# Optimization experiments

Hardware: AMD Instinct MI355X
Metric: run time of the kernel (lower is better)

The kernel has to match this reference:

```python
import jax, jax.numpy as jnp
import numpy as np
from jax import lax

EPS = 1e-6


def layernorm2d(x, w, b):
    # channel LayerNorm over dim C of NCHW (biased variance), matching LayerNormFunction
    mu = jnp.mean(x, axis=1, keepdims=True)
    var = jnp.mean((x - mu) ** 2, axis=1, keepdims=True)
    y = (x - mu) * lax.rsqrt(var + EPS)
    return w[None, :, None, None] * y + b[None, :, None, None]


def conv1x1(x, W, b):
    # x: (N,C,H,W), W: (O,C), b: (O,)
    return jnp.einsum('nchw,oc->nohw', x, W) + b[None, :, None, None]


def conv3x3(x, W, b):
    # W: (O,I,3,3)
    y = lax.conv_general_dilated(x, W, window_strides=(1, 1), padding='SAME',
                                 dimension_numbers=('NCHW', 'OIHW', 'NCHW'))
    return y + b[None, :, None, None]


def avg_pool3x3(x):
    # torch F.avg_pool2d k=3, s=1, p=1, count_include_pad=True -> always divide by 9
    s = lax.reduce_window(x, 0.0, lax.add, (1, 1, 3, 3), (1, 1, 1, 1),
                          [(0, 0), (0, 0), (1, 1), (1, 1)])
    return s / 9.0


def setup_inputs() -> dict:
    key = jax.random.key(0)
    N, C, H, W = 8, 64, 128, 256
    ks = jax.random.split(key, 12)
    d = {
        'x_l': jax.random.normal(ks[0], (N, C, H, W), jnp.float32),
        'x_r': jax.random.normal(ks[1], (N, C, H, W), jnp.float32),
        'nl_w': jnp.ones((C,), jnp.float32),
        'nl_b': jnp.zeros((C,), jnp.float32),
        'nr_w': jnp.ones((C,), jnp.float32),
        'nr_b': jnp.zeros((C,), jnp.float32),
        'Wq_l': jax.random.normal(ks[2], (C, C), jnp.float32) * 0.05,
        'bq_l': jax.random.normal(ks[3], (C,), jnp.float32) * 0.05,
        'Wq_r': jax.random.normal(ks[4], (C, C), jnp.float32) * 0.05,
        'bq_r': jax.random.normal(ks[5], (C,), jnp.float32) * 0.05,
        'Wv_r': jax.random.normal(ks[6], (C, C), jnp.float32) * 0.05,
        'bv_r': jax.random.normal(ks[7], (C,), jnp.float32) * 0.05,
        'beta': jax.random.normal(ks[8], (1, C, 1, 1), jnp.float32) * 0.1,
        'gamma': jax.random.normal(ks[9], (1, C, 1, 1), jnp.float32) * 0.1,
        'W_hf': jax.random.normal(ks[10], (C, C, 3, 3), jnp.float32) * 0.02,
        'b_hf': jax.random.normal(ks[11], (C,), jnp.float32) * 0.02,
    }
    return d


def reference(x_l, x_r, nl_w, nl_b, nr_w, nr_b, Wq_l, bq_l, Wq_r, bq_r,
              Wv_r, bv_r, beta, gamma, W_hf, b_hf):
    C = x_l.shape[1]
    scale = C ** (-0.5)

    # Projections (1x1 convs); Q_l, Q_r, V_r as (N,H,W,C)
    Q_l = jnp.transpose(conv1x1(layernorm2d(x_l, nl_w, nl_b), Wq_l, bq_l), (0, 2, 3, 1))
    Q_r = jnp.transpose(conv1x1(layernorm2d(x_r, nr_w, nr_b), Wq_r, bq_r), (0, 2, 3, 1))
    V_r = jnp.transpose(conv1x1(x_r, Wv_r, bv_r), (0, 2, 3, 1))

    # Per-scanline cross attention: (N,H,W,W)
    attn = jnp.einsum('nhwc,nhvc->nhwv', Q_l, Q_r) * scale
    attn = jax.nn.softmax(attn, axis=-1)
    F_r2l = jnp.einsum('nhwv,nhvc->nhwc', attn, V_r)  # (N,H,W,C)
    F_r2l = jnp.transpose(F_r2l, (0, 3, 1, 2)) * beta  # (N,C,H,W)

    # High-frequency branch
    hf = conv3x3(x_r - avg_pool3x3(x_r), W_hf, b_hf)

    return x_l + F_r2l + gamma * hf
```

## Files before the change

### kernel.cpp

```cpp
#include <hip/hip_runtime.h>
#include <hip/hip_bf16.h>

#define N_ 8
#define C_ 64
#define H_ 128
#define W_ 256
#define HW_ (H_*W_)
#define CHW_ (C_*H_*W_)

typedef unsigned int u32;
typedef unsigned short u16;
typedef float f32x4 __attribute__((ext_vector_type(4)));
typedef short bf16x8 __attribute__((ext_vector_type(8)));

__device__ __forceinline__ float blo(u32 u) { return __uint_as_float(u << 16); }
__device__ __forceinline__ float bhi(u32 u) { return __uint_as_float(u & 0xffff0000u); }
__device__ __forceinline__ u16 f2bf(float f) {
    u32 u = __float_as_uint(f);
    u32 lsb = (u >> 16) & 1u;
    u += 0x7fffu + lsb;
    return (u16)(u >> 16);
}
__device__ __forceinline__ u32 pack2(float a, float b) {
    return (u32)f2bf(a) | ((u32)f2bf(b) << 16);
}
__device__ __forceinline__ int rmap(int px) {
    return (px & 0xF8) | ((px + (px >> 3)) & 7);
}

__global__ __launch_bounds__(512, 2) void k_fused(
    const float* __restrict__ xl, const float* __restrict__ xr,
    const float* __restrict__ nlw, const float* __restrict__ nlb,
    const float* __restrict__ nrw, const float* __restrict__ nrb,
    const float* __restrict__ Wql, const float* __restrict__ bql,
    const float* __restrict__ Wqr, const float* __restrict__ bqr,
    const float* __restrict__ Wvr, const float* __restrict__ bvr,
    const float* __restrict__ beta, float* __restrict__ out)
{
    __shared__ u32 B1[8192];
    __shared__ u32 B2[8192];
    __shared__ float muA[256], rsA[256];
    __shared__ float SlA[64], BlA[64], SrA[64], BrA[64], BvA[64];
    const int tid  = threadIdx.x;
    const int lane = tid & 63, wv = tid >> 6;
    const int l15  = lane & 15, kg = lane >> 4;
    const int mw   = wv & 3;
    const int nh   = wv >> 2;
    const int blk  = blockIdx.x;
    const int n = blk >> 7, h = blk & 127;
    const size_t gbase = (size_t)n*CHW_ + (size_t)h*W_;

    if (tid < 64) {
        const int o = tid;
        float sl = 0.f, bl = bql[o], sr = 0.f, br = bqr[o];
        for (int c = 0; c < 64; ++c) {
            float wl = Wql[o*64+c], wr = Wqr[o*64+c];
            sl += wl * nlw[c];
            bl += wl * nlb[c];
            sr += wr * nrw[c];
            br += wr * nrb[c];
        }
        SlA[o] = sl; BlA[o] = bl; SrA[o] = sr; BrA[o] = br; BvA[o] = bvr[o];
    }

    const int oA = mw*16 + l15;
    bf16x8 aL[2], aR[2], aV[2];
    #pragma unroll
    for (int hf = 0; hf < 2; ++hf) {
        bf16x8 tl, tr, tv;
        #pragma unroll
        for (int j = 0; j < 8; ++j) {
            const int c = hf*32 + kg*8 + j;
            tl[j] = (short)f2bf(Wql[oA*64+c] * nlw[c]);
            tr[j] = (short)f2bf(Wqr[oA*64+c] * nrw[c]);
            tv[j] = (short)f2bf(Wvr[oA*64+c]);
        }
        aL[hf] = tl; aR[hf] = tr; aV[hf] = tv;
    }

    const int schunk = tid >> 6;
    const int sj     = tid & 63;

    {
        const int c0 = schunk*8;
        float4 v[8];
        #pragma unroll
        for (int e = 0; e < 8; ++e)
            v[e] = *(const float4*)(xl + gbase + (size_t)(c0+e)*HW_ + sj*4);
        #pragma unroll
        for (int t = 0; t < 4; ++t) {
            const int px = sj*4 + t;
            const int r = rmap(px);
            u32 q0,q1,q2,q3;
            const float* f0 = (const float*)&v[0]; const float* f1 = (const float*)&v[1];
            const float* f2 = (const float*)&v[2]; const float* f3 = (const float*)&v[3];
            const float* f4 = (const float*)&v[4]; const float* f5 = (const float*)&v[5];
            const float* f6 = (const float*)&v[6]; const float* f7 = (const float*)&v[7];
            asm("v_cvt_pk_bf16_f32 %0, %1, %2" : "=v"(q0) : "v"(f0[t]), "v"(f1[t]));
            asm("v_cvt_pk_bf16_f32 %0, %1, %2" : "=v"(q1) : "v"(f2[t]), "v"(f3[t]));
            asm("v_cvt_pk_bf16_f32 %0, %1, %2" : "=v"(q2) : "v"(f4[t]), "v"(f5[t]));
            asm("v_cvt_pk_bf16_f32 %0, %1, %2" : "=v"(q3) : "v"(f6[t]), "v"(f7[t]));
            uint4 pv; pv.x=q0; pv.y=q1; pv.z=q2; pv.w=q3;
            *(uint4*)&B1[r*32 + ((schunk ^ (r&7))<<2)] = pv;
        }
    }
    float4 vr2[8];
    {
        const int c0 = schunk*8;
        #pragma unroll
        for (int e = 0; e < 8; ++e)
            vr2[e] = *(const float4*)(xr + gbase + (size_t)(c0+e)*HW_ + sj*4);
    }
    __syncthreads();
    if (tid < 256) {
        const int px = tid;
        const int r = rmap(px);
        float sum = 0.f, ssq = 0.f;
        #pragma unroll
        for (int c8 = 0; c8 < 8; ++c8) {
            uint4 val = *(const uint4*)&B1[r*32 + ((c8 ^ (r&7))<<2)];
            const u32* wp = (const u32*)&val;
            #pragma unroll
            for (int q = 0; q < 4; ++q) {
                float a = blo(wp[q]), b = bhi(wp[q]);
                sum += a + b; ssq += a*a + b*b;
            }
        }
        float mu = sum * (1.f/64.f);
        float var = ssq * (1.f/64.f) - mu*mu;
        muA[px] = mu;
        rsA[px] = rsqrtf(var + 1e-6f);
    }
    __syncthreads();
    {
        float Sv[4], Bv[4];
        #pragma unroll
        for (int r4 = 0; r4 < 4; ++r4) {
            Sv[r4] = SlA[mw*16 + kg*4 + r4];
            Bv[r4] = BlA[mw*16 + kg*4 + r4];
        }
        #pragma unroll
        for (int nt2 = 0; nt2 < 8; ++nt2) {
            const int nt = nh*8 + nt2;
            const int px = nt*16 + l15;
            const int r = rmap(px);
            f32x4 d = {0.f,0.f,0.f,0.f};
            #pragma unroll
            for (int hf = 0; hf < 2; ++hf) {
                bf16x8 b = *(const bf16x8*)&B1[r*32 + (((hf*4+kg) ^ (r&7))<<2)];
                d = __builtin_amdgcn_mfma_f32_16x16x32_bf16(aL[hf], b, d, 0, 0, 0);
            }
            const float mu = muA[px], rs = rsA[px];
            uint2 pv;
            pv.x = pack2(rs*(d[0] - mu*Sv[0]) + Bv[0], rs*(d[1] - mu*Sv[1]) + Bv[1]);
            pv.y = pack2(rs*(d[2] - mu*Sv[2]) + Bv[2], rs*(d[3] - mu*Sv[3]) + Bv[3]);
            const int ci = (mw*2 + (kg>>1)) ^ (px & 7);
            *(uint2*)&B2[px*32 + (ci<<2) + (kg&1)*2] = pv;
        }
    }
    __syncthreads();

    bf16x8 qf[2][2];
    #pragma unroll
    for (int ntq = 0; ntq < 2; ++ntq)
        #pragma unroll
        for (int ci = 0; ci < 2; ++ci) {
            const int q = wv*32 + ntq*16 + l15;
            qf[ntq][ci] = *(const bf16x8*)&B2[q*32 + (((ci*4+kg) ^ (q&7))<<2)];
        }
    {
        #pragma unroll
        for (int t = 0; t < 4; ++t) {
            const int px = sj*4 + t;
            const int r = rmap(px);
            u32 q0,q1,q2,q3;
            const float* f0 = (const float*)&vr2[0]; const float* f1 = (const float*)&vr2[1];
            const float* f2 = (const float*)&vr2[2]; const float* f3 = (const float*)&vr2[3];
            const float* f4 = (const float*)&vr2[4]; const float* f5 = (const float*)&vr2[5];
            const float* f6 = (const float*)&vr2[6]; const float* f7 = (const float*)&vr2[7];
            asm("v_cvt_pk_bf16_f32 %0, %1, %2" : "=v"(q0) : "v"(f0[t]), "v"(f1[t]));
            asm("v_cvt_pk_bf16_f32 %0, %1, %2" : "=v"(q1) : "v"(f2[t]), "v"(f3[t]));
            asm("v_cvt_pk_bf16_f32 %0, %1, %2" : "=v"(q2) : "v"(f4[t]), "v"(f5[t]));
            asm("v_cvt_pk_bf16_f32 %0, %1, %2" : "=v"(q3) : "v"(f6[t]), "v"(f7[t]));
            uint4 pv; pv.x=q0; pv.y=q1; pv.z=q2; pv.w=q3;
            *(uint4*)&B1[r*32 + ((schunk ^ (r&7))<<2)] = pv;
        }
    }
    __syncthreads();
    if (tid < 256) {
        const int px = tid;
        const int r = rmap(px);
        float sum = 0.f, ssq = 0.f;
        #pragma unroll
        for (int c8 = 0; c8 < 8; ++c8) {
            uint4 val = *(const uint4*)&B1[r*32 + ((c8 ^ (r&7))<<2)];
            const u32* wp = (const u32*)&val;
            #pragma unroll
            for (int q = 0; q < 4; ++q) {
                float a = blo(wp[q]), b = bhi(wp[q]);
                sum += a + b; ssq += a*a + b*b;
            }
        }
        float mu = sum * (1.f/64.f);
        float var = ssq * (1.f/64.f) - mu*mu;
        muA[px] = mu;
        rsA[px] = rsqrtf(var + 1e-6f);
    }
    __syncthreads();

    u32 hq[8][2], hv[8][2];
    {
        float Sv[4], Bv[4];
        #pragma unroll
        for (int r4 = 0; r4 < 4; ++r4) {
            Sv[r4] = SrA[mw*16 + kg*4 + r4];
            Bv[r4] = BrA[mw*16 + kg*4 + r4];
        }
        const int chv = mw*16 + l15;
        const float vbias = BvA[chv];
        #pragma unroll
        for (int nt2 = 0; nt2 < 8; ++nt2) {
            const int nt = nh*8 + nt2;
            const int px = nt*16 + l15;
            const int r = rmap(px);
            bf16x8 bX[2];
            #pragma unroll
            for (int hf = 0; hf < 2; ++hf)
                bX[hf] = *(const bf16x8*)&B1[r*32 + (((hf*4+kg) ^ (r&7))<<2)];
            f32x4 dq = {0.f,0.f,0.f,0.f};
            f32x4 dv = {0.f,0.f,0.f,0.f};
            #pragma unroll
            for (int hf = 0; hf < 2; ++hf) {
                dq = __builtin_amdgcn_mfma_f32_16x16x32_bf16(aR[hf], bX[hf], dq, 0, 0, 0);
                dv = __builtin_amdgcn_mfma_f32_16x16x32_bf16(bX[hf], aV[hf], dv, 0, 0, 0);
            }
            const float mu = muA[px], rs = rsA[px];
            hq[nt2][0] = pack2(rs*(dq[0] - mu*Sv[0]) + Bv[0], rs*(dq[1] - mu*Sv[1]) + Bv[1]);
            hq[nt2][1] = pack2(rs*(dq[2] - mu*Sv[2]) + Bv[2], rs*(dq[3] - mu*Sv[3]) + Bv[3]);
            hv[nt2][0] = pack2(dv[0] + vbias, dv[1] + vbias);
            hv[nt2][1] = pack2(dv[2] + vbias, dv[3] + vbias);
        }
    }
    __syncthreads();
    {
        const int chv = mw*16 + l15;
        u16* Vts16 = (u16*)B2;
        #pragma unroll
        for (int nt2 = 0; nt2 < 8; ++nt2) {
            const int nt = nh*8 + nt2;
            const int px = nt*16 + l15;
            const int ciq = (mw*2 + (kg>>1)) ^ (px & 7);
            uint2 pq; pq.x = hq[nt2][0]; pq.y = hq[nt2][1];
            *(uint2*)&B1[px*32 + (ciq<<2) + (kg&1)*2] = pq;
            uint2 pw; pw.x = hv[nt2][0]; pw.y = hv[nt2][1];
            const int swz = (nt*2 + (kg>>1)) ^ (chv & 7);
            *(uint2*)&Vts16[chv*256 + (swz<<3) + (kg&1)*4] = pw;
        }
    }
    __syncthreads();

    f32x4 oacc[2][4];
    #pragma unroll
    for (int a = 0; a < 2; ++a)
        #pragma unroll
        for (int b = 0; b < 4; ++b)
            oacc[a][b] = (f32x4){0.f,0.f,0.f,0.f};
    float lsum[2] = {0.f,0.f};
    const uint4* KsR = (const uint4*)B1;
    const u16* Vts = (const u16*)B2;
    const int srcA = ((2*kg) & 3)*16 + l15;

    for (int kb = 0; kb < 8; ++kb) {
        f32x4 st[2][2];
        #pragma unroll
        for (int mt = 0; mt < 2; ++mt)
            #pragma unroll
            for (int nt = 0; nt < 2; ++nt)
                st[mt][nt] = (f32x4){0.f,0.f,0.f,0.f};
        #pragma unroll
        for (int ci = 0; ci < 2; ++ci) {
            bf16x8 a0 = *(const bf16x8*)&KsR[(kb*32 +      l15)*8 + ((ci*4 + kg) ^ (l15 & 7))];
            bf16x8 a1 = *(const bf16x8*)&KsR[(kb*32 + 16 + l15)*8 + ((ci*4 + kg) ^ (l15 & 7))];
            #pragma unroll
            for (int nt = 0; nt < 2; ++nt) {
                st[0][nt] = __builtin_amdgcn_mfma_f32_16x16x32_bf16(a0, qf[nt][ci], st[0][nt], 0, 0, 0);
                st[1][nt] = __builtin_amdgcn_mfma_f32_16x16x32_bf16(a1, qf[nt][ci], st[1][nt], 0, 0, 0);
            }
        }
        bf16x8 paR[2];
        #pragma unroll
        for (int nt = 0; nt < 2; ++nt) {
            float p00 = __expf(st[0][nt][0]*0.125f);
            float p01 = __expf(st[0][nt][1]*0.125f);
            float p02 = __expf(st[0][nt][2]*0.125f);
            float p03 = __expf(st[0][nt][3]*0.125f);
            float p10 = __expf(st[1][nt][0]*0.125f);
            float p11 = __expf(st[1][nt][1]*0.125f);
            float p12 = __expf(st[1][nt][2]*0.125f);
            float p13 = __expf(st[1][nt][3]*0.125f);
            lsum[nt] += ((p00+p01)+(p02+p03)) + ((p10+p11)+(p12+p13));
            u32 pk00, pk01, pk10, pk11;
            asm("v_cvt_pk_bf16_f32 %0, %1, %2" : "=v"(pk00) : "v"(p00), "v"(p01));
            asm("v_cvt_pk_bf16_f32 %0, %1, %2" : "=v"(pk01) : "v"(p02), "v"(p03));
            asm("v_cvt_pk_bf16_f32 %0, %1, %2" : "=v"(pk10) : "v"(p10), "v"(p11));
            asm("v_cvt_pk_bf16_f32 %0, %1, %2" : "=v"(pk11) : "v"(p12), "v"(p13));
            int a00 = __shfl((int)pk00, srcA, 64);
            int a01 = __shfl((int)pk01, srcA, 64);
            int a10 = __shfl((int)pk10, srcA, 64);
            int a11 = __shfl((int)pk11, srcA, 64);
            int b00 = __shfl((int)pk00, srcA + 16, 64);
            int b01 = __shfl((int)pk01, srcA + 16, 64);
            int b10 = __shfl((int)pk10, srcA + 16, 64);
            int b11 = __shfl((int)pk11, srcA + 16, 64);
            const bool lo = (kg < 2);
            union { u32 u[4]; bf16x8 v; } pu;
            pu.u[0] = (u32)(lo ? a00 : a10);
            pu.u[1] = (u32)(lo ? a01 : a11);
            pu.u[2] = (u32)(lo ? b00 : b10);
            pu.u[3] = (u32)(lo ? b01 : b11);
            paR[nt] = pu.v;
        }
        bf16x8 vb[4];
        #pragma unroll
        for (int nc = 0; nc < 4; ++nc)
            vb[nc] = *(const bf16x8*)&Vts[(nc*16 + l15)*256 + ((kb*4 + kg) ^ (l15 & 7))*8];
        #pragma unroll
        for (int qt = 0; qt < 2; ++qt)
            #pragma unroll
            for (int nc = 0; nc < 4; ++nc)
                oacc[qt][nc] = __builtin_amdgcn_mfma_f32_16x16x32_bf16(paR[qt], vb[nc], oacc[qt][nc], 0, 0, 0);
    }

    #pragma unroll
    for (int nt = 0; nt < 2; ++nt) {
        float s = lsum[nt];
        s += __shfl_xor(s, 16, 64);
        s += __shfl_xor(s, 32, 64);
        lsum[nt] = s;
    }
    float linv[2][4];
    #pragma unroll
    for (int qt = 0; qt < 2; ++qt)
        #pragma unroll
        for (int r = 0; r < 4; ++r)
            linv[qt][r] = 1.0f / __shfl(lsum[qt], kg*4 + r, 64);

    const size_t qbase = gbase + wv*32;
    #pragma unroll
    for (int nc = 0; nc < 4; ++nc) {
        const int ch = nc*16 + l15;
        const float bch = beta[ch];
        #pragma unroll
        for (int qt = 0; qt < 2; ++qt) {
            const size_t gidx = qbase + (size_t)ch*HW_ + qt*16 + kg*4;
            f32x4 x4 = *(const f32x4*)&xl[gidx];
            f32x4 vals;
            #pragma unroll
            for (int r = 0; r < 4; ++r)
                vals[r] = x4[r] + bch*(oacc[qt][nc][r]*linv[qt][r]);
            *(f32x4*)&out[gidx] = vals;
        }
    }
}

__global__ __launch_bounds__(256) void k_hipass(
    const float* __restrict__ xr, u16* __restrict__ Tt)
{
    __shared__ u16 Ts[64*256];
    const int bid = blockIdx.x;
    const int blk = (bid & 7)*128 + (bid >> 3);
    const int n = blk >> 7, h = blk & 127;
    const int tid = threadIdx.x;
    const int lane = tid & 63, wv = tid >> 6;
    const float* rowp = xr + (size_t)n*CHW_ + (size_t)h*W_ + lane*4;

    #pragma unroll
    for (int ci = 0; ci < 16; ++ci) {
        const int c = wv*16 + ci;
        const float* pc = rowp + (size_t)c*HW_;
        float ctr0=0.f, ctr1=0.f, ctr2=0.f, ctr3=0.f;
        float s0=0.f, s1=0.f, s2=0.f, s3=0.f;
        #pragma unroll
        for (int dy = -1; dy <= 1; ++dy) {
            const int hh = h + dy;
            float4 v = {0.f,0.f,0.f,0.f};
            if (hh >= 0 && hh < 128) v = *(const float4*)(pc + dy*W_);
            float lft = __shfl_up(v.w, 1);
            float rgt = __shfl_down(v.x, 1);
            if (lane == 0)  lft = 0.f;
            if (lane == 63) rgt = 0.f;
            s0 += lft + v.x + v.y;
            s1 += v.x + v.y + v.z;
            s2 += v.y + v.z + v.w;
            s3 += v.z + v.w + rgt;
            if (dy == 0) { ctr0=v.x; ctr1=v.y; ctr2=v.z; ctr3=v.w; }
        }
        uint2 pv;
        pv.x = pack2(ctr0 - s0*(1.f/9.f), ctr1 - s1*(1.f/9.f));
        pv.y = pack2(ctr2 - s2*(1.f/9.f), ctr3 - s3*(1.f/9.f));
        const int swz = (c >> 3) << 3;
        *(uint2*)&Ts[c*256 + ((lane*4) ^ swz)] = pv;
    }
    __syncthreads();
    uint4* gout = (uint4*)(Tt + (size_t)blk*256*64);
    #pragma unroll
    for (int iter = 0; iter < 8; ++iter) {
        const int lin = iter*256 + tid;
        const int px = lin >> 3, chunk = lin & 7;
        const int pxs = px ^ (chunk << 3);
        u32 w4[4];
        #pragma unroll
        for (int tp = 0; tp < 4; ++tp) {
            const int c0 = chunk*8 + tp*2;
            u16 a = Ts[(c0    )*256 + pxs];
            u16 b = Ts[(c0 + 1)*256 + pxs];
            w4[tp] = (u32)a | ((u32)b << 16);
        }
        uint4 v; v.x=w4[0]; v.y=w4[1]; v.z=w4[2]; v.w=w4[3];
        gout[lin] = v;
    }
}

__device__ __forceinline__ void conv_tile(
    const uint4* __restrict__ buf, const bf16x8* A,
    const float* gv, const float* bv,
    int n, int h, int w0, int mt, int l15, int kg,
    float* __restrict__ out)
{
    f32x4 acc[4] = {{0,0,0,0},{0,0,0,0},{0,0,0,0},{0,0,0,0}};
    #pragma unroll
    for (int s = 0; s < 18; ++s) {
        const int q  = s >> 1;
        const int dy = q / 3, dx = q % 3;
        const int c0 = (s & 1)*4 + kg;
        #pragma unroll
        for (int nt = 0; nt < 4; ++nt) {
            const int wt = nt*16 + l15 + dx;
            bf16x8 b = *(const bf16x8*)&buf[(dy*66 + wt)*8 + (c0 ^ (wt & 7))];
            acc[nt] = __builtin_amdgcn_mfma_f32_16x16x32_bf16(A[s], b, acc[nt], 0, 0, 0);
        }
    }
    #pragma unroll
    for (int nt = 0; nt < 4; ++nt) {
        const int px = w0 + nt*16 + l15;
        #pragma unroll
        for (int r = 0; r < 4; ++r) {
            const int oo = mt*16 + kg*4 + r;
            size_t idx = (size_t)(n*64 + oo)*HW_ + (size_t)h*W_ + px;
            out[idx] += gv[r]*(acc[nt][r] + bv[r]);
        }
    }
}

__global__ __launch_bounds__(256) void k_conv(
    const u16* __restrict__ Tt, const float* __restrict__ Whf,
    const float* __restrict__ bhf, const float* __restrict__ gam,
    float* __restrict__ out)
{
    __shared__ uint4 Xs[2][1584];
    const int tid  = threadIdx.x;
    const int lane = tid & 63;
    const int mt   = tid >> 6;
    const int l15  = lane & 15;
    const int kg   = lane >> 4;
    const int bid  = blockIdx.x;
    const int blk2 = (bid & 7)*256 + (bid >> 3);
    const int row  = blk2 >> 1, half = blk2 & 1;
    const int n = row >> 7, h = row & 127;
    const int w00 = half*128;
    const int w01 = w00 + 64;

    const int oa = mt*16 + l15;
    bf16x8 A[18];
    #pragma unroll
    for (int s = 0; s < 18; ++s) {
        const int q  = s >> 1;
        const int ib = (s & 1)*32 + kg*8;
        bf16x8 a;
        #pragma unroll
        for (int j = 0; j < 8; ++j) {
            float wv = Whf[(size_t)(oa*64 + ib + j)*9 + q];
            a[j] = (short)f2bf(wv);
        }
        A[s] = a;
    }
    float gv[4], bv[4];
    #pragma unroll
    for (int r = 0; r < 4; ++r) {
        int oo = mt*16 + kg*4 + r;
        gv[r] = gam[oo];
        bv[r] = bhf[oo];
    }

    for (int it = tid; it < 1584; it += 256) {
        int dy    = it / 528;
        int rem   = it - dy*528;
        int wt    = rem >> 3;
        int chunk = rem & 7;
        int hh = h + dy - 1;
        int wg = w00 + wt - 1;
        uint4 v = {0,0,0,0};
        if (hh >= 0 && hh < 128 && wg >= 0 && wg < 256)
            v = *(const uint4*)(Tt + (((size_t)(n*128 + hh)*256 + wg)*64 + chunk*8));
        Xs[0][(dy*66 + wt)*8 + (chunk ^ (wt & 7))] = v;
    }
    __syncthreads();

    uint4 rr[7];
    #pragma unroll
    for (int k = 0; k < 7; ++k) {
        const int it = k*256 + tid;
        if (it < 1584) {
            int dy    = it / 528;
            int rem   = it - dy*528;
            int wt    = rem >> 3;
            int chunk = rem & 7;
            int hh = h + dy - 1;
            int wg = w01 + wt - 1;
            uint4 v = {0,0,0,0};
            if (hh >= 0 && hh < 128 && wg >= 0 && wg < 256)
                v = *(const uint4*)(Tt + (((size_t)(n*128 + hh)*256 + wg)*64 + chunk*8));
            rr[k] = v;
        }
    }

    conv_tile(&Xs[0][0], A, gv, bv, n, h, w00, mt, l15, kg, out);

    #pragma unroll
    for (int k = 0; k < 7; ++k) {
        const int it = k*256 + tid;
        if (it < 1584) {
            int dy    = it / 528;
            int rem   = it - dy*528;
            int wt    = rem >> 3;
            int chunk = rem & 7;
            Xs[1][(dy*66 + wt)*8 + (chunk ^ (wt & 7))] = rr[k];
        }
    }
    __syncthreads();
    conv_tile(&Xs[1][0], A, gv, bv, n, h, w01, mt, l15, kg, out);
}

extern "C" void kernel_launch(void* const* d_in, const int* in_sizes, int n_in,
                              void* d_out, int out_size, void* d_ws, size_t ws_size,
                              hipStream_t stream)
{
    const float* xl   = (const float*)d_in[0];
    const float* xr   = (const float*)d_in[1];
    const float* nlw  = (const float*)d_in[2];
    const float* nlb  = (const float*)d_in[3];
    const float* nrw  = (const float*)d_in[4];
    const float* nrb  = (const float*)d_in[5];
    const float* Wql  = (const float*)d_in[6];
    const float* bql  = (const float*)d_in[7];
    const float* Wqr  = (const float*)d_in[8];
    const float* bqr  = (const float*)d_in[9];
    const float* Wvr  = (const float*)d_in[10];
    const float* bvr  = (const float*)d_in[11];
    const float* beta = (const float*)d_in[12];
    const float* gam  = (const float*)d_in[13];
    const float* Whf  = (const float*)d_in[14];
    const float* bhf  = (const float*)d_in[15];
    float* out = (float*)d_out;

    u16* Tt = (u16*)d_ws;

    k_hipass<<<1024, 256, 0, stream>>>(xr, Tt);
    k_fused<<<1024, 512, 0, stream>>>(xl, xr, nlw, nlb, nrw, nrb,
                                      Wql, bql, Wqr, bqr, Wvr, bvr,
                                      beta, out);
    k_conv<<<2048, 256, 0, stream>>>(Tt, Whf, bhf, gam, out);
}
```

Before: 175.0 us.

## Double fused attention block to 1024 threads, halving per-thread work

The fused per-scanline attention kernel now launches 1024 threads per block instead of 512. Each thread loads 4 channels instead of 8, each wave handles 4 pixel tiles in the projection phases, and each wave owns 16 query rows instead of 32 in the attention loop. This cuts per-thread register pressure and adds more waves to hide latency. The cost is that each K/V fragment loaded from shared memory now feeds half as many MFMAs, and occupancy is capped at one block per CU by the launch bounds.

```diff
diff --git a/kernel.cpp b/kernel.cpp
--- a/kernel.cpp
+++ b/kernel.cpp
@@ -28,7 +28,7 @@
     return (px & 0xF8) | ((px + (px >> 3)) & 7);
 }
 
-__global__ __launch_bounds__(512, 2) void k_fused(
+__global__ __launch_bounds__(1024, 1) void k_fused(
     const float* __restrict__ xl, const float* __restrict__ xr,
     const float* __restrict__ nlw, const float* __restrict__ nlb,
     const float* __restrict__ nrw, const float* __restrict__ nrb,
@@ -78,37 +78,35 @@
         aL[hf] = tl; aR[hf] = tr; aV[hf] = tv;
     }
 
-    const int schunk = tid >> 6;
+    const int chunk4 = tid >> 6;
+    const int schunk = chunk4 >> 1;
+    const int ssub   = chunk4 & 1;
     const int sj     = tid & 63;
 
     {
-        const int c0 = schunk*8;
-        float4 v[8];
-        #pragma unroll
-        for (int e = 0; e < 8; ++e)
+        const int c0 = chunk4*4;
+        float4 v[4];
+        #pragma unroll
+        for (int e = 0; e < 4; ++e)
             v[e] = *(const float4*)(xl + gbase + (size_t)(c0+e)*HW_ + sj*4);
         #pragma unroll
         for (int t = 0; t < 4; ++t) {
             const int px = sj*4 + t;
             const int r = rmap(px);
-            u32 q0,q1,q2,q3;
+            u32 q0,q1;
             const float* f0 = (const float*)&v[0]; const float* f1 = (const float*)&v[1];
             const float* f2 = (const float*)&v[2]; const float* f3 = (const float*)&v[3];
-            const float* f4 = (const float*)&v[4]; const float* f5 = (const float*)&v[5];
-            const float* f6 = (const float*)&v[6]; const float* f7 = (const float*)&v[7];
             asm("v_cvt_pk_bf16_f32 %0, %1, %2" : "=v"(q0) : "v"(f0[t]), "v"(f1[t]));
             asm("v_cvt_pk_bf16_f32 %0, %1, %2" : "=v"(q1) : "v"(f2[t]), "v"(f3[t]));
-            asm("v_cvt_pk_bf16_f32 %0, %1, %2" : "=v"(q2) : "v"(f4[t]), "v"(f5[t]));
-            asm("v_cvt_pk_bf16_f32 %0, %1, %2" : "=v"(q3) : "v"(f6[t]), "v"(f7[t]));
-            uint4 pv; pv.x=q0; pv.y=q1; pv.z=q2; pv.w=q3;
-            *(uint4*)&B1[r*32 + ((schunk ^ (r&7))<<2)] = pv;
-        }
-    }
-    float4 vr2[8];
-    {
-        const int c0 = schunk*8;
-        #pragma unroll
-        for (int e = 0; e < 8; ++e)
+            uint2 pv; pv.x=q0; pv.y=q1;
+            *(uint2*)&B1[r*32 + ((schunk ^ (r&7))<<2) + ssub*2] = pv;
+        }
+    }
+    float4 vr2[4];
+    {
+        const int c0 = chunk4*4;
+        #pragma unroll
+        for (int e = 0; e < 4; ++e)
             vr2[e] = *(const float4*)(xr + gbase + (size_t)(c0+e)*HW_ + sj*4);
     }
     __syncthreads();
@@ -140,8 +138,8 @@
             Bv[r4] = BlA[mw*16 + kg*4 + r4];
         }
         #pragma unroll
-        for (int nt2 = 0; nt2 < 8; ++nt2) {
-            const int nt = nh*8 + nt2;
+        for (int nt2 = 0; nt2 < 4; ++nt2) {
+            const int nt = nh*4 + nt2;
             const int px = nt*16 + l15;
             const int r = rmap(px);
             f32x4 d = {0.f,0.f,0.f,0.f};
@@ -160,30 +158,24 @@
     }
     __syncthreads();
 
-    bf16x8 qf[2][2];
-    #pragma unroll
-    for (int ntq = 0; ntq < 2; ++ntq)
-        #pragma unroll
-        for (int ci = 0; ci < 2; ++ci) {
-            const int q = wv*32 + ntq*16 + l15;
-            qf[ntq][ci] = *(const bf16x8*)&B2[q*32 + (((ci*4+kg) ^ (q&7))<<2)];
-        }
+    bf16x8 qf[2];
+    #pragma unroll
+    for (int ci = 0; ci < 2; ++ci) {
+        const int q = wv*16 + l15;
+        qf[ci] = *(const bf16x8*)&B2[q*32 + (((ci*4+kg) ^ (q&7))<<2)];
+    }
     {
         #pragma unroll
         for (int t = 0; t < 4; ++t) {
             const int px = sj*4 + t;
             const int r = rmap(px);
-            u32 q0,q1,q2,q3;
+            u32 q0,q1;
             const float* f0 = (const float*)&vr2[0]; const float* f1 = (const float*)&vr2[1];
             const float* f2 = (const float*)&vr2[2]; const float* f3 = (const float*)&vr2[3];
-            const float* f4 = (const float*)&vr2[4]; const float* f5 = (const float*)&vr2[5];
-            const float* f6 = (const float*)&vr2[6]; const float* f7 = (const float*)&vr2[7];
             asm("v_cvt_pk_bf16_f32 %0, %1, %2" : "=v"(q0) : "v"(f0[t]), "v"(f1[t]));
             asm("v_cvt_pk_bf16_f32 %0, %1, %2" : "=v"(q1) : "v"(f2[t]), "v"(f3[t]));
-            asm("v_cvt_pk_bf16_f32 %0, %1, %2" : "=v"(q2) : "v"(f4[t]), "v"(f5[t]));
-            asm("v_cvt_pk_bf16_f32 %0, %1, %2" : "=v"(q3) : "v"(f6[t]), "v"(f7[t]));
-            uint4 pv; pv.x=q0; pv.y=q1; pv.z=q2; pv.w=q3;
-            *(uint4*)&B1[r*32 + ((schunk ^ (r&7))<<2)] = pv;
+            uint2 pv; pv.x=q0; pv.y=q1;
+            *(uint2*)&B1[r*32 + ((schunk ^ (r&7))<<2) + ssub*2] = pv;
         }
     }
     __syncthreads();
@@ -208,7 +200,7 @@
     }
     __syncthreads();
 
-    u32 hq[8][2], hv[8][2];
+    u32 hq[4][2], hv[4][2];
     {
         float Sv[4], Bv[4];
         #pragma unroll
@@ -219,8 +211,8 @@
         const int chv = mw*16 + l15;
         const float vbias = BvA[chv];
         #pragma unroll
-        for (int nt2 = 0; nt2 < 8; ++nt2) {
-            const int nt = nh*8 + nt2;
+        for (int nt2 = 0; nt2 < 4; ++nt2) {
+            const int nt = nh*4 + nt2;
             const int px = nt*16 + l15;
             const int r = rmap(px);
             bf16x8 bX[2];
@@ -246,8 +238,8 @@
         const int chv = mw*16 + l15;
         u16* Vts16 = (u16*)B2;
         #pragma unroll
-        for (int nt2 = 0; nt2 < 8; ++nt2) {
-            const int nt = nh*8 + nt2;
+        for (int nt2 = 0; nt2 < 4; ++nt2) {
+            const int nt = nh*4 + nt2;
             const int px = nt*16 + l15;
             const int ciq = (mw*2 + (kg>>1)) ^ (px & 7);
             uint2 pq; pq.x = hq[nt2][0]; pq.y = hq[nt2][1];
@@ -259,46 +251,37 @@
     }
     __syncthreads();
 
-    f32x4 oacc[2][4];
-    #pragma unroll
-    for (int a = 0; a < 2; ++a)
-        #pragma unroll
-        for (int b = 0; b < 4; ++b)
-            oacc[a][b] = (f32x4){0.f,0.f,0.f,0.f};
-    float lsum[2] = {0.f,0.f};
+    f32x4 oacc[4];
+    #pragma unroll
+    for (int b = 0; b < 4; ++b)
+        oacc[b] = (f32x4){0.f,0.f,0.f,0.f};
+    float lsum = 0.f;
     const uint4* KsR = (const uint4*)B1;
     const u16* Vts = (const u16*)B2;
     const int srcA = ((2*kg) & 3)*16 + l15;
 
     for (int kb = 0; kb < 8; ++kb) {
-        f32x4 st[2][2];
-        #pragma unroll
-        for (int mt = 0; mt < 2; ++mt)
-            #pragma unroll
-            for (int nt = 0; nt < 2; ++nt)
-                st[mt][nt] = (f32x4){0.f,0.f,0.f,0.f};
+        f32x4 st[2];
+        st[0] = (f32x4){0.f,0.f,0.f,0.f};
+        st[1] = (f32x4){0.f,0.f,0.f,0.f};
         #pragma unroll
         for (int ci = 0; ci < 2; ++ci) {
             bf16x8 a0 = *(const bf16x8*)&KsR[(kb*32 +      l15)*8 + ((ci*4 + kg) ^ (l15 & 7))];
             bf16x8 a1 = *(const bf16x8*)&KsR[(kb*32 + 16 + l15)*8 + ((ci*4 + kg) ^ (l15 & 7))];
-            #pragma unroll
-            for (int nt = 0; nt < 2; ++nt) {
-                st[0][nt] = __builtin_amdgcn_mfma_f32_16x16x32_bf16(a0, qf[nt][ci], st[0][nt], 0, 0, 0);
-                st[1][nt] = __builtin_amdgcn_mfma_f32_16x16x32_bf16(a1, qf[nt][ci], st[1][nt], 0, 0, 0);
-            }
-        }
-        bf16x8 paR[2];
-        #pragma unroll
-        for (int nt = 0; nt < 2; ++nt) {
-            float p00 = __expf(st[0][nt][0]*0.125f);
-            float p01 = __expf(st[0][nt][1]*0.125f);
-            float p02 = __expf(st[0][nt][2]*0.125f);
-            float p03 = __expf(st[0][nt][3]*0.125f);
-            float p10 = __expf(st[1][nt][0]*0.125f);
-            float p11 = __expf(st[1][nt][1]*0.125f);
-            float p12 = __expf(st[1][nt][2]*0.125f);
-            float p13 = __expf(st[1][nt][3]*0.125f);
-            lsum[nt] += ((p00+p01)+(p02+p03)) + ((p10+p11)+(p12+p13));
+            st[0] = __builtin_amdgcn_mfma_f32_16x16x32_bf16(a0, qf[ci], st[0], 0, 0, 0);
+            st[1] = __builtin_amdgcn_mfma_f32_16x16x32_bf16(a1, qf[ci], st[1], 0, 0, 0);
+        }
+        bf16x8 paR;
+        {
+            float p00 = __expf(st[0][0]*0.125f);
+            float p01 = __expf(st[0][1]*0.125f);
+            float p02 = __expf(st[0][2]*0.125f);
+            float p03 = __expf(st[0][3]*0.125f);
+            float p10 = __expf(st[1][0]*0.125f);
+            float p11 = __expf(st[1][1]*0.125f);
+            float p12 = __expf(st[1][2]*0.125f);
+            float p13 = __expf(st[1][3]*0.125f);
+            lsum += ((p00+p01)+(p02+p03)) + ((p10+p11)+(p12+p13));
             u32 pk00, pk01, pk10, pk11;
             asm("v_cvt_pk_bf16_f32 %0, %1, %2" : "=v"(pk00) : "v"(p00), "v"(p01));
             asm("v_cvt_pk_bf16_f32 %0, %1, %2" : "=v"(pk01) : "v"(p02), "v"(p03));
@@ -318,48 +301,40 @@
             pu.u[1] = (u32)(lo ? a01 : a11);
             pu.u[2] = (u32)(lo ? b00 : b10);
             pu.u[3] = (u32)(lo ? b01 : b11);
-            paR[nt] = pu.v;
+            paR = pu.v;
         }
         bf16x8 vb[4];
         #pragma unroll
         for (int nc = 0; nc < 4; ++nc)
             vb[nc] = *(const bf16x8*)&Vts[(nc*16 + l15)*256 + ((kb*4 + kg) ^ (l15 & 7))*8];
         #pragma unroll
-        for (int qt = 0; qt < 2; ++qt)
-            #pragma unroll
-            for (int nc = 0; nc < 4; ++nc)
-                oacc[qt][nc] = __builtin_amdgcn_mfma_f32_16x16x32_bf16(paR[qt], vb[nc], oacc[qt][nc], 0, 0, 0);
-    }
-
-    #pragma unroll
-    for (int nt = 0; nt < 2; ++nt) {
-        float s = lsum[nt];
+        for (int nc = 0; nc < 4; ++nc)
+            oacc[nc] = __builtin_amdgcn_mfma_f32_16x16x32_bf16(paR, vb[nc], oacc[nc], 0, 0, 0);
+    }
+
+    {
+        float s = lsum;
         s += __shfl_xor(s, 16, 64);
         s += __shfl_xor(s, 32, 64);
-        lsum[nt] = s;
-    }
-    float linv[2][4];
-    #pragma unroll
-    for (int qt = 0; qt < 2; ++qt)
-        #pragma unroll
-        for (int r = 0; r < 4; ++r)
-            linv[qt][r] = 1.0f / __shfl(lsum[qt], kg*4 + r, 64);
-
-    const size_t qbase = gbase + wv*32;
+        lsum = s;
+    }
+    float linv[4];
+    #pragma unroll
+    for (int r = 0; r < 4; ++r)
+        linv[r] = 1.0f / __shfl(lsum, kg*4 + r, 64);
+
+    const size_t qbase = gbase + wv*16;
     #pragma unroll
     for (int nc = 0; nc < 4; ++nc) {
         const int ch = nc*16 + l15;
         const float bch = beta[ch];
-        #pragma unroll
-        for (int qt = 0; qt < 2; ++qt) {
-            const size_t gidx = qbase + (size_t)ch*HW_ + qt*16 + kg*4;
-            f32x4 x4 = *(const f32x4*)&xl[gidx];
-            f32x4 vals;
-            #pragma unroll
-            for (int r = 0; r < 4; ++r)
-                vals[r] = x4[r] + bch*(oacc[qt][nc][r]*linv[qt][r]);
-            *(f32x4*)&out[gidx] = vals;
-        }
+        const size_t gidx = qbase + (size_t)ch*HW_ + kg*4;
+        f32x4 x4 = *(const f32x4*)&xl[gidx];
+        f32x4 vals;
+        #pragma unroll
+        for (int r = 0; r < 4; ++r)
+            vals[r] = x4[r] + bch*(oacc[nc][r]*linv[r]);
+        *(f32x4*)&out[gidx] = vals;
     }
 }
 
@@ -566,8 +541,8 @@
     u16* Tt = (u16*)d_ws;
 
     k_hipass<<<1024, 256, 0, stream>>>(xr, Tt);
-    k_fused<<<1024, 512, 0, stream>>>(xl, xr, nlw, nlb, nrw, nrb,
-                                      Wql, bql, Wqr, bqr, Wvr, bvr,
-                                      beta, out);
+    k_fused<<<1024, 1024, 0, stream>>>(xl, xr, nlw, nlb, nrw, nrb,
+                                       Wql, bql, Wqr, bqr, Wvr, bvr,
+                                       beta, out);
     k_conv<<<2048, 256, 0, stream>>>(Tt, Whf, bhf, gam, out);
 }
```

Result: slower. 222.8 us (+27.4%).
